# Kernel optimization log

Measured on AMD Instinct MI355X. Metric: run time of the kernel, lower is better.

## Reference

```python
import jax, jax.numpy as jnp
import numpy as np

N_NODES = 50000


def gcn_conv(x, src, dst, W, b, num_nodes):
    """PyG GCNConv: y = D^{-1/2} (A + I) D^{-1/2} (x @ W) + b.
    src/dst already include self-loops."""
    h = x @ W  # [N, F_out]
    deg = jax.ops.segment_sum(jnp.ones_like(dst, dtype=h.dtype), dst,
                              num_segments=num_nodes)  # in-degree incl. self-loop
    dinv = jnp.where(deg > 0, jax.lax.rsqrt(deg), 0.0)
    norm = dinv[src] * dinv[dst]  # [E]
    msgs = h[src] * norm[:, None]  # gather + scale, [E, F_out]
    out = jax.ops.segment_sum(msgs, dst, num_segments=num_nodes)
    return out + b


def setup_inputs() -> dict:
    key = jax.random.key(0)
    k1, k2, k3, k4 = jax.random.split(key, 4)
    latent, hidden, out_ch = 64, 128, 64
    n_edges = 800000
    z = jax.random.normal(k1, (N_NODES, latent), dtype=jnp.float32)
    edge_index = jax.random.randint(k2, (2, n_edges), 0, N_NODES, dtype=jnp.int64)
    # Glorot-style scaled weights
    W1 = jax.random.normal(k3, (latent, hidden), dtype=jnp.float32) * (1.0 / np.sqrt(latent))
    b1 = jnp.zeros((hidden,), dtype=jnp.float32)
    W2 = jax.random.normal(k4, (hidden, out_ch), dtype=jnp.float32) * (1.0 / np.sqrt(hidden))
    b2 = jnp.zeros((out_ch,), dtype=jnp.float32)
    return {"z": z, "edge_index": edge_index, "W1": W1, "b1": b1, "W2": W2, "b2": b2}


def reference(z, edge_index, W1, b1, W2, b2):
    num_nodes = z.shape[0]
    loops = jnp.arange(num_nodes, dtype=edge_index.dtype)
    src = jnp.concatenate([edge_index[0], loops])  # add self-loops
    dst = jnp.concatenate([edge_index[1], loops])
    x = gcn_conv(z, src, dst, W1, b1, num_nodes)
    x = jax.nn.relu(x)
    x = gcn_conv(x, src, dst, W2, b2, num_nodes)
    x = jax.nn.relu(x)
    return x
```

## Files before the change

### kernel.cpp

```cpp
#include <hip/hip_runtime.h>
#include <hip/hip_fp16.h>

static inline size_t align256(size_t x){ return (x + 255) & ~(size_t)255; }

#define CAP 64
#define NPART 8

__device__ __forceinline__ int detect_is64(const unsigned* __restrict__ e){
  unsigned v = e[2 * (threadIdx.x & 63) + 1];
  return (__ballot(v != 0u) == 0ull) ? 1 : 0;
}

__device__ __forceinline__ int load_idx(const void* edges, long i, int is64){
  return is64 ? (int)((const long long*)edges)[i] : ((const int*)edges)[i];
}

__global__ __launch_bounds__(256) void build_kernel(const void* __restrict__ edges, int E,
                                                    int* __restrict__ cnt,
                                                    unsigned short* __restrict__ csr,
                                                    int N){
  const int is64 = detect_is64((const unsigned*)edges);
  const int p  = blockIdx.x & (NPART - 1);
  const int q  = blockIdx.x >> 3;
  const int nq = gridDim.x >> 3;
  const int nper = (N + NPART - 1) / NPART;
  const int lo = p * nper;
  const int hi = min(lo + nper, N);
  const int stride = nq * 256;
  for (int i = q * 256 + threadIdx.x; i < E; i += stride){
    const int d = load_idx(edges, (long)E + i, is64);
    if (d < lo || d >= hi) continue;
    const int s = load_idx(edges, i, is64);
    const int pos = atomicAdd(&cnt[d], 1);
    if (pos < CAP) csr[((size_t)d << 6) + pos] = (unsigned short)s;
  }
}

__device__ __forceinline__ float4 h4_to_f4(uint2 r){
  const __half2 a = *(const __half2*)&r.x;
  const __half2 b = *(const __half2*)&r.y;
  const float2 fa = __half22float2(a);
  const float2 fb = __half22float2(b);
  return make_float4(fa.x, fa.y, fb.x, fb.y);
}

__device__ __forceinline__ uint2 f4_to_h4(float4 v){
  uint2 r;
  const __half2 a = __float22half2_rn(make_float2(v.x, v.y));
  const __half2 b = __float22half2_rn(make_float2(v.z, v.w));
  r.x = *(const unsigned*)&a;
  r.y = *(const unsigned*)&b;
  return r;
}

__global__ __launch_bounds__(256) void prep_kernel(const float4* __restrict__ z,
                                                   uint2* __restrict__ zh,
                                                   const int* __restrict__ cnt,
                                                   float* __restrict__ dinv, int N){
  const int idx = blockIdx.x * 256 + threadIdx.x;
  const int node = idx >> 4;
  if (node >= N) return;
  const float di = rsqrtf((float)(cnt[node] + 1));
  if ((idx & 15) == 0) dinv[node] = di;
  const float4 v = z[idx];
  zh[idx] = f4_to_h4(make_float4(di * v.x, di * v.y, di * v.z, di * v.w));
}

__device__ __forceinline__ float4 gather_sum_h(const uint2* __restrict__ H,
                                               const unsigned short* __restrict__ row,
                                               int deg, int j, float4 acc){
  int e = 0;
  #pragma unroll 1
  for (; e + 4 <= deg; e += 4){
    const ushort4 rr = *(const ushort4*)(row + e);
    const float4 v0 = h4_to_f4(H[(size_t)rr.x * 16 + j]);
    const float4 v1 = h4_to_f4(H[(size_t)rr.y * 16 + j]);
    const float4 v2 = h4_to_f4(H[(size_t)rr.z * 16 + j]);
    const float4 v3 = h4_to_f4(H[(size_t)rr.w * 16 + j]);
    acc.x += (v0.x + v1.x) + (v2.x + v3.x);
    acc.y += (v0.y + v1.y) + (v2.y + v3.y);
    acc.z += (v0.z + v1.z) + (v2.z + v3.z);
    acc.w += (v0.w + v1.w) + (v2.w + v3.w);
  }
  #pragma unroll 1
  for (; e < deg; ++e){
    const float4 v = h4_to_f4(H[(size_t)row[e] * 16 + j]);
    acc.x += v.x; acc.y += v.y; acc.z += v.z; acc.w += v.w;
  }
  return acc;
}

__global__ __launch_bounds__(512) void agg_gemm1_kernel(const uint2* __restrict__ zh,
                                                        const unsigned short* __restrict__ csr,
                                                        const int* __restrict__ cnt,
                                                        const float* __restrict__ dinv,
                                                        const float* __restrict__ W1,
                                                        const float* __restrict__ b1,
                                                        float* __restrict__ x1, int N){
  __shared__ float Wl[64 * 128];
  __shared__ float rows[32 * 64];
  const int t = threadIdx.x;

  {
    const float4* Wg = (const float4*)W1;
    float4* Wd = (float4*)Wl;
    #pragma unroll
    for (int i = 0; i < 4; ++i) Wd[t + i * 512] = Wg[t + i * 512];
  }

  const int local = t >> 4;
  const int j = t & 15;
  const int node = blockIdx.x * 32 + local;
  float4 acc = make_float4(0.f, 0.f, 0.f, 0.f);
  if (node < N){
    const float di = dinv[node];
    acc = h4_to_f4(zh[(size_t)node * 16 + j]);
    const int deg = min(cnt[node], CAP);
    acc = gather_sum_h(zh, csr + ((size_t)node << 6), deg, j, acc);
    acc = make_float4(di * acc.x, di * acc.y, di * acc.z, di * acc.w);
  }
  ((float4*)rows)[local * 16 + j] = acc;
  __syncthreads();

  const int jc = t & 127;
  const int g = t >> 7;
  const float bv = b1[jc];
  float accv[8];
  #pragma unroll
  for (int n = 0; n < 8; ++n) accv[n] = bv;

  #pragma unroll 2
  for (int k4 = 0; k4 < 16; ++k4){
    const float w0 = Wl[(4 * k4 + 0) * 128 + jc];
    const float w1 = Wl[(4 * k4 + 1) * 128 + jc];
    const float w2 = Wl[(4 * k4 + 2) * 128 + jc];
    const float w3 = Wl[(4 * k4 + 3) * 128 + jc];
    #pragma unroll
    for (int n = 0; n < 8; ++n){
      const float4 r = ((const float4*)rows)[(g * 8 + n) * 16 + k4];
      accv[n] = fmaf(r.x, w0, accv[n]);
      accv[n] = fmaf(r.y, w1, accv[n]);
      accv[n] = fmaf(r.z, w2, accv[n]);
      accv[n] = fmaf(r.w, w3, accv[n]);
    }
  }

  #pragma unroll
  for (int n = 0; n < 8; ++n){
    const int nn = blockIdx.x * 32 + g * 8 + n;
    if (nn < N) x1[(size_t)nn * 128 + jc] = fmaxf(accv[n], 0.0f);
  }
}

__global__ __launch_bounds__(256) void agg2_kernel(const uint2* __restrict__ X,
                                                   float4* __restrict__ Y,
                                                   const unsigned short* __restrict__ csr,
                                                   const int* __restrict__ cnt,
                                                   const float* __restrict__ dinv,
                                                   const float4* __restrict__ bias,
                                                   int N){
  const int local = threadIdx.x >> 4;
  const int j = threadIdx.x & 15;
  const int node = blockIdx.x * 16 + local;
  if (node >= N) return;
  const float di = dinv[node];
  float4 acc = h4_to_f4(X[(size_t)node * 16 + j]);
  const int deg = min(cnt[node], CAP);
  acc = gather_sum_h(X, csr + ((size_t)node << 6), deg, j, acc);
  const float4 b = bias[j];
  float4 o;
  o.x = fmaxf(fmaf(di, acc.x, b.x), 0.f);
  o.y = fmaxf(fmaf(di, acc.y, b.y), 0.f);
  o.z = fmaxf(fmaf(di, acc.z, b.z), 0.f);
  o.w = fmaxf(fmaf(di, acc.w, b.w), 0.f);
  Y[(size_t)node * 16 + j] = o;
}

__global__ __launch_bounds__(256) void gemm2_kernel(const float* __restrict__ X,
                                                    const float* __restrict__ W,
                                                    const float* __restrict__ dinv,
                                                    __half* __restrict__ Y, int N){
  constexpr int FIN = 128, FOUT = 64, NT = 32;
  constexpr int G = 256 / FOUT;
  constexpr int NTG = NT / G;
  __shared__ float Wl[FIN * FOUT];
  __shared__ float rows[NT * FIN];
  const int t = threadIdx.x;
  const int node0 = blockIdx.x * NT;

  {
    const float4* Wg = (const float4*)W;
    float4* Wd = (float4*)Wl;
    #pragma unroll
    for (int i = 0; i < FIN * FOUT / 4 / 256; ++i) Wd[t + i * 256] = Wg[t + i * 256];
  }
  {
    float4* rd = (float4*)rows;
    const float4* Xg = (const float4*)X;
    constexpr int TOT = NT * FIN / 4;
    #pragma unroll
    for (int i = 0; i < TOT / 256; ++i){
      const int id = t + i * 256;
      const int n = id / (FIN / 4);
      const int k4 = id % (FIN / 4);
      int node = node0 + n; if (node > N - 1) node = N - 1;
      rd[id] = Xg[(size_t)node * (FIN / 4) + k4];
    }
  }
  __syncthreads();

  const int j = t % FOUT;
  const int g = t / FOUT;
  float acc[NTG];
  #pragma unroll
  for (int n = 0; n < NTG; ++n) acc[n] = 0.0f;

  #pragma unroll 2
  for (int k4 = 0; k4 < FIN / 4; ++k4){
    const float w0 = Wl[(4 * k4 + 0) * FOUT + j];
    const float w1 = Wl[(4 * k4 + 1) * FOUT + j];
    const float w2 = Wl[(4 * k4 + 2) * FOUT + j];
    const float w3 = Wl[(4 * k4 + 3) * FOUT + j];
    #pragma unroll
    for (int n = 0; n < NTG; ++n){
      const float4 r = ((const float4*)rows)[(g * NTG + n) * (FIN / 4) + k4];
      acc[n] = fmaf(r.x, w0, acc[n]);
      acc[n] = fmaf(r.y, w1, acc[n]);
      acc[n] = fmaf(r.z, w2, acc[n]);
      acc[n] = fmaf(r.w, w3, acc[n]);
    }
  }

  #pragma unroll
  for (int n = 0; n < NTG; ++n){
    const int node = node0 + g * NTG + n;
    if (node < N) Y[(size_t)node * FOUT + j] = __float2half(acc[n] * dinv[node]);
  }
}

extern "C" void kernel_launch(void* const* d_in, const int* in_sizes, int n_in,
                              void* d_out, int out_size, void* d_ws, size_t ws_size,
                              hipStream_t stream){
  const float* z  = (const float*)d_in[0];
  const void*  edges = d_in[1];
  const float* W1 = (const float*)d_in[2];
  const float* b1 = (const float*)d_in[3];
  const float* W2 = (const float*)d_in[4];
  const float* b2 = (const float*)d_in[5];
  float* out = (float*)d_out;

  constexpr int F0 = 64, F1 = 128;
  const int N = in_sizes[0] / F0;
  const int E = in_sizes[1] / 2;
  (void)n_in; (void)out_size;

  char* p = (char*)d_ws;
  int*            cnt  = (int*)p;            p += align256((size_t)N * 4);
  float*          dinv = (float*)p;          p += align256((size_t)N * 4);
  unsigned short* csr  = (unsigned short*)p; p += align256((size_t)N * CAP * 2);
  __half*         hbuf = (__half*)p;         p += align256((size_t)N * F0 * 2);
  float*          x1   = (float*)p;          p += align256((size_t)N * F1 * 4);
  (void)ws_size;
  __half* zh = hbuf;
  __half* h2 = hbuf;

  hipMemsetAsync(cnt, 0, (size_t)N * 4, stream);
  build_kernel<<<1024, 256, 0, stream>>>(edges, E, cnt, csr, N);
  prep_kernel<<<(N * 16 + 255) / 256, 256, 0, stream>>>(
      (const float4*)z, (uint2*)zh, cnt, dinv, N);

  agg_gemm1_kernel<<<(N + 31) / 32, 512, 0, stream>>>(
      (const uint2*)zh, csr, cnt, dinv, W1, b1, x1, N);

  gemm2_kernel<<<(N + 31) / 32, 256, 0, stream>>>(x1, W2, dinv, h2, N);
  agg2_kernel<<<(N + 15) / 16, 256, 0, stream>>>(
      (const uint2*)h2, (float4*)out, csr, cnt, dinv, (const float4*)b2, N);
}
```

Measured before the change: 202.8 us.

## Pack edges into 32-bit words and widen gathers to 16-byte loads

A new pack kernel reads the int64 edge list once and writes packed (dst<<16|src) 32-bit words, also zeroing the counts in place of a separate memset. The partitioned build kernel then rereads this compact array eight times instead of the wide int64 edges. The aggregation kernels now use 8 lanes per node with uint4 (8 half) loads instead of 16 lanes with uint2, and gemm1 processes 64 nodes per block. The packing assumes node ids fit in 16 bits and adds one extra kernel launch plus a workspace buffer.

```diff
diff --git a/kernel.cpp b/kernel.cpp
--- a/kernel.cpp
+++ b/kernel.cpp
@@ -15,11 +15,24 @@
   return is64 ? (int)((const long long*)edges)[i] : ((const int*)edges)[i];
 }
 
-__global__ __launch_bounds__(256) void build_kernel(const void* __restrict__ edges, int E,
+__global__ __launch_bounds__(256) void pack_kernel(const void* __restrict__ edges, int E,
+                                                   unsigned* __restrict__ pe,
+                                                   int* __restrict__ cnt, int N){
+  const int is64 = detect_is64((const unsigned*)edges);
+  const int t0 = blockIdx.x * 256 + threadIdx.x;
+  const int stride = gridDim.x * 256;
+  for (int i = t0; i < N; i += stride) cnt[i] = 0;
+  for (int i = t0; i < E; i += stride){
+    const unsigned s = (unsigned)load_idx(edges, i, is64);
+    const unsigned d = (unsigned)load_idx(edges, (long)E + i, is64);
+    pe[i] = (d << 16) | (s & 0xFFFFu);
+  }
+}
+
+__global__ __launch_bounds__(256) void build_kernel(const unsigned* __restrict__ pe, int E,
                                                     int* __restrict__ cnt,
                                                     unsigned short* __restrict__ csr,
                                                     int N){
-  const int is64 = detect_is64((const unsigned*)edges);
   const int p  = blockIdx.x & (NPART - 1);
   const int q  = blockIdx.x >> 3;
   const int nq = gridDim.x >> 3;
@@ -28,69 +41,64 @@
   const int hi = min(lo + nper, N);
   const int stride = nq * 256;
   for (int i = q * 256 + threadIdx.x; i < E; i += stride){
-    const int d = load_idx(edges, (long)E + i, is64);
+    const unsigned v = pe[i];
+    const int d = (int)(v >> 16);
     if (d < lo || d >= hi) continue;
-    const int s = load_idx(edges, i, is64);
     const int pos = atomicAdd(&cnt[d], 1);
-    if (pos < CAP) csr[((size_t)d << 6) + pos] = (unsigned short)s;
-  }
-}
-
-__device__ __forceinline__ float4 h4_to_f4(uint2 r){
-  const __half2 a = *(const __half2*)&r.x;
-  const __half2 b = *(const __half2*)&r.y;
-  const float2 fa = __half22float2(a);
-  const float2 fb = __half22float2(b);
-  return make_float4(fa.x, fa.y, fb.x, fb.y);
-}
-
-__device__ __forceinline__ uint2 f4_to_h4(float4 v){
-  uint2 r;
-  const __half2 a = __float22half2_rn(make_float2(v.x, v.y));
-  const __half2 b = __float22half2_rn(make_float2(v.z, v.w));
-  r.x = *(const unsigned*)&a;
-  r.y = *(const unsigned*)&b;
-  return r;
-}
-
-__global__ __launch_bounds__(256) void prep_kernel(const float4* __restrict__ z,
-                                                   uint2* __restrict__ zh,
-                                                   const int* __restrict__ cnt,
-                                                   float* __restrict__ dinv, int N){
-  const int idx = blockIdx.x * 256 + threadIdx.x;
-  const int node = idx >> 4;
-  if (node >= N) return;
-  const float di = rsqrtf((float)(cnt[node] + 1));
-  if ((idx & 15) == 0) dinv[node] = di;
-  const float4 v = z[idx];
-  zh[idx] = f4_to_h4(make_float4(di * v.x, di * v.y, di * v.z, di * v.w));
-}
-
-__device__ __forceinline__ float4 gather_sum_h(const uint2* __restrict__ H,
-                                               const unsigned short* __restrict__ row,
-                                               int deg, int j, float4 acc){
+    if (pos < CAP) csr[((size_t)d << 6) + pos] = (unsigned short)(v & 0xFFFFu);
+  }
+}
+
+__device__ __forceinline__ void h8_acc(uint4 r, float* a){
+  const __half2* h = (const __half2*)&r;
+  #pragma unroll
+  for (int k = 0; k < 4; ++k){
+    const float2 f = __half22float2(h[k]);
+    a[2*k]     += f.x;
+    a[2*k + 1] += f.y;
+  }
+}
+
+__device__ __forceinline__ void gather8(const uint4* __restrict__ H,
+                                        const unsigned short* __restrict__ row,
+                                        int deg, int j, float* a){
   int e = 0;
   #pragma unroll 1
   for (; e + 4 <= deg; e += 4){
     const ushort4 rr = *(const ushort4*)(row + e);
-    const float4 v0 = h4_to_f4(H[(size_t)rr.x * 16 + j]);
-    const float4 v1 = h4_to_f4(H[(size_t)rr.y * 16 + j]);
-    const float4 v2 = h4_to_f4(H[(size_t)rr.z * 16 + j]);
-    const float4 v3 = h4_to_f4(H[(size_t)rr.w * 16 + j]);
-    acc.x += (v0.x + v1.x) + (v2.x + v3.x);
-    acc.y += (v0.y + v1.y) + (v2.y + v3.y);
-    acc.z += (v0.z + v1.z) + (v2.z + v3.z);
-    acc.w += (v0.w + v1.w) + (v2.w + v3.w);
+    const uint4 v0 = H[(size_t)rr.x * 8 + j];
+    const uint4 v1 = H[(size_t)rr.y * 8 + j];
+    const uint4 v2 = H[(size_t)rr.z * 8 + j];
+    const uint4 v3 = H[(size_t)rr.w * 8 + j];
+    h8_acc(v0, a); h8_acc(v1, a); h8_acc(v2, a); h8_acc(v3, a);
   }
   #pragma unroll 1
-  for (; e < deg; ++e){
-    const float4 v = h4_to_f4(H[(size_t)row[e] * 16 + j]);
-    acc.x += v.x; acc.y += v.y; acc.z += v.z; acc.w += v.w;
-  }
-  return acc;
-}
-
-__global__ __launch_bounds__(512) void agg_gemm1_kernel(const uint2* __restrict__ zh,
+  for (; e < deg; ++e) h8_acc(H[(size_t)row[e] * 8 + j], a);
+}
+
+__global__ __launch_bounds__(256) void prep_kernel(const float4* __restrict__ z,
+                                                   uint4* __restrict__ zh,
+                                                   const int* __restrict__ cnt,
+                                                   float* __restrict__ dinv, int N){
+  const int idx = blockIdx.x * 256 + threadIdx.x;
+  const int node = idx >> 3;
+  if (node >= N) return;
+  const int j = idx & 7;
+  const float di = rsqrtf((float)(cnt[node] + 1));
+  if (j == 0) dinv[node] = di;
+  const float4 v0 = z[(size_t)node * 16 + j * 2];
+  const float4 v1 = z[(size_t)node * 16 + j * 2 + 1];
+  const __half2 a0 = __float22half2_rn(make_float2(di * v0.x, di * v0.y));
+  const __half2 a1 = __float22half2_rn(make_float2(di * v0.z, di * v0.w));
+  const __half2 a2 = __float22half2_rn(make_float2(di * v1.x, di * v1.y));
+  const __half2 a3 = __float22half2_rn(make_float2(di * v1.z, di * v1.w));
+  uint4 r;
+  r.x = *(const unsigned*)&a0; r.y = *(const unsigned*)&a1;
+  r.z = *(const unsigned*)&a2; r.w = *(const unsigned*)&a3;
+  zh[idx] = r;
+}
+
+__global__ __launch_bounds__(512) void agg_gemm1_kernel(const uint4* __restrict__ zh,
                                                         const unsigned short* __restrict__ csr,
                                                         const int* __restrict__ cnt,
                                                         const float* __restrict__ dinv,
@@ -98,7 +106,7 @@
                                                         const float* __restrict__ b1,
                                                         float* __restrict__ x1, int N){
   __shared__ float Wl[64 * 128];
-  __shared__ float rows[32 * 64];
+  __shared__ float rows[64 * 64];
   const int t = threadIdx.x;
 
   {
@@ -108,26 +116,29 @@
     for (int i = 0; i < 4; ++i) Wd[t + i * 512] = Wg[t + i * 512];
   }
 
-  const int local = t >> 4;
-  const int j = t & 15;
-  const int node = blockIdx.x * 32 + local;
-  float4 acc = make_float4(0.f, 0.f, 0.f, 0.f);
+  const int local = t >> 3;
+  const int j = t & 7;
+  const int node = blockIdx.x * 64 + local;
+  float a[8] = {0.f, 0.f, 0.f, 0.f, 0.f, 0.f, 0.f, 0.f};
   if (node < N){
+    h8_acc(zh[(size_t)node * 8 + j], a);
+    const int deg = min(cnt[node], CAP);
+    gather8(zh, csr + ((size_t)node << 6), deg, j, a);
     const float di = dinv[node];
-    acc = h4_to_f4(zh[(size_t)node * 16 + j]);
-    const int deg = min(cnt[node], CAP);
-    acc = gather_sum_h(zh, csr + ((size_t)node << 6), deg, j, acc);
-    acc = make_float4(di * acc.x, di * acc.y, di * acc.z, di * acc.w);
-  }
-  ((float4*)rows)[local * 16 + j] = acc;
+    #pragma unroll
+    for (int k = 0; k < 8; ++k) a[k] *= di;
+  }
+  float4* rp = (float4*)&rows[t * 8];
+  rp[0] = make_float4(a[0], a[1], a[2], a[3]);
+  rp[1] = make_float4(a[4], a[5], a[6], a[7]);
   __syncthreads();
 
   const int jc = t & 127;
   const int g = t >> 7;
   const float bv = b1[jc];
-  float accv[8];
-  #pragma unroll
-  for (int n = 0; n < 8; ++n) accv[n] = bv;
+  float accv[16];
+  #pragma unroll
+  for (int n = 0; n < 16; ++n) accv[n] = bv;
 
   #pragma unroll 2
   for (int k4 = 0; k4 < 16; ++k4){
@@ -136,8 +147,8 @@
     const float w2 = Wl[(4 * k4 + 2) * 128 + jc];
     const float w3 = Wl[(4 * k4 + 3) * 128 + jc];
     #pragma unroll
-    for (int n = 0; n < 8; ++n){
-      const float4 r = ((const float4*)rows)[(g * 8 + n) * 16 + k4];
+    for (int n = 0; n < 16; ++n){
+      const float4 r = ((const float4*)rows)[(g * 16 + n) * 16 + k4];
       accv[n] = fmaf(r.x, w0, accv[n]);
       accv[n] = fmaf(r.y, w1, accv[n]);
       accv[n] = fmaf(r.z, w2, accv[n]);
@@ -146,34 +157,41 @@
   }
 
   #pragma unroll
-  for (int n = 0; n < 8; ++n){
-    const int nn = blockIdx.x * 32 + g * 8 + n;
+  for (int n = 0; n < 16; ++n){
+    const int nn = blockIdx.x * 64 + g * 16 + n;
     if (nn < N) x1[(size_t)nn * 128 + jc] = fmaxf(accv[n], 0.0f);
   }
 }
 
-__global__ __launch_bounds__(256) void agg2_kernel(const uint2* __restrict__ X,
+__global__ __launch_bounds__(256) void agg2_kernel(const uint4* __restrict__ X,
                                                    float4* __restrict__ Y,
                                                    const unsigned short* __restrict__ csr,
                                                    const int* __restrict__ cnt,
                                                    const float* __restrict__ dinv,
                                                    const float4* __restrict__ bias,
                                                    int N){
-  const int local = threadIdx.x >> 4;
-  const int j = threadIdx.x & 15;
-  const int node = blockIdx.x * 16 + local;
+  const int local = threadIdx.x >> 3;
+  const int j = threadIdx.x & 7;
+  const int node = blockIdx.x * 32 + local;
   if (node >= N) return;
+  float a[8] = {0.f, 0.f, 0.f, 0.f, 0.f, 0.f, 0.f, 0.f};
+  h8_acc(X[(size_t)node * 8 + j], a);
+  const int deg = min(cnt[node], CAP);
+  gather8(X, csr + ((size_t)node << 6), deg, j, a);
   const float di = dinv[node];
-  float4 acc = h4_to_f4(X[(size_t)node * 16 + j]);
-  const int deg = min(cnt[node], CAP);
-  acc = gather_sum_h(X, csr + ((size_t)node << 6), deg, j, acc);
-  const float4 b = bias[j];
-  float4 o;
-  o.x = fmaxf(fmaf(di, acc.x, b.x), 0.f);
-  o.y = fmaxf(fmaf(di, acc.y, b.y), 0.f);
-  o.z = fmaxf(fmaf(di, acc.z, b.z), 0.f);
-  o.w = fmaxf(fmaf(di, acc.w, b.w), 0.f);
-  Y[(size_t)node * 16 + j] = o;
+  const float4 b0 = bias[j * 2];
+  const float4 b1v = bias[j * 2 + 1];
+  float4 o0, o1;
+  o0.x = fmaxf(fmaf(di, a[0], b0.x), 0.f);
+  o0.y = fmaxf(fmaf(di, a[1], b0.y), 0.f);
+  o0.z = fmaxf(fmaf(di, a[2], b0.z), 0.f);
+  o0.w = fmaxf(fmaf(di, a[3], b0.w), 0.f);
+  o1.x = fmaxf(fmaf(di, a[4], b1v.x), 0.f);
+  o1.y = fmaxf(fmaf(di, a[5], b1v.y), 0.f);
+  o1.z = fmaxf(fmaf(di, a[6], b1v.z), 0.f);
+  o1.w = fmaxf(fmaf(di, a[7], b1v.w), 0.f);
+  Y[(size_t)node * 16 + j * 2] = o0;
+  Y[(size_t)node * 16 + j * 2 + 1] = o1;
 }
 
 __global__ __launch_bounds__(256) void gemm2_kernel(const float* __restrict__ X,
@@ -258,21 +276,22 @@
   int*            cnt  = (int*)p;            p += align256((size_t)N * 4);
   float*          dinv = (float*)p;          p += align256((size_t)N * 4);
   unsigned short* csr  = (unsigned short*)p; p += align256((size_t)N * CAP * 2);
+  unsigned*       pe   = (unsigned*)p;       p += align256((size_t)E * 4);
   __half*         hbuf = (__half*)p;         p += align256((size_t)N * F0 * 2);
   float*          x1   = (float*)p;          p += align256((size_t)N * F1 * 4);
   (void)ws_size;
   __half* zh = hbuf;
   __half* h2 = hbuf;
 
-  hipMemsetAsync(cnt, 0, (size_t)N * 4, stream);
-  build_kernel<<<1024, 256, 0, stream>>>(edges, E, cnt, csr, N);
-  prep_kernel<<<(N * 16 + 255) / 256, 256, 0, stream>>>(
-      (const float4*)z, (uint2*)zh, cnt, dinv, N);
-
-  agg_gemm1_kernel<<<(N + 31) / 32, 512, 0, stream>>>(
-      (const uint2*)zh, csr, cnt, dinv, W1, b1, x1, N);
+  pack_kernel<<<1024, 256, 0, stream>>>(edges, E, pe, cnt, N);
+  build_kernel<<<1024, 256, 0, stream>>>(pe, E, cnt, csr, N);
+  prep_kernel<<<(N * 8 + 255) / 256, 256, 0, stream>>>(
+      (const float4*)z, (uint4*)zh, cnt, dinv, N);
+
+  agg_gemm1_kernel<<<(N + 63) / 64, 512, 0, stream>>>(
+      (const uint4*)zh, csr, cnt, dinv, W1, b1, x1, N);
 
   gemm2_kernel<<<(N + 31) / 32, 256, 0, stream>>>(x1, W2, dinv, h2, N);
-  agg2_kernel<<<(N + 15) / 16, 256, 0, stream>>>(
-      (const uint2*)h2, (float4*)out, csr, cnt, dinv, (const float4*)b2, N);
-}
+  agg2_kernel<<<(N + 31) / 32, 256, 0, stream>>>(
+      (const uint4*)h2, (float4*)out, csr, cnt, dinv, (const float4*)b2, N);
+}
```

Measured after the change: 199.8 us. About the same (-1.5%).
